# Kernel tuning notes

Hardware: AMD Instinct MI355X
Metric: run time of the kernel (lower is better)

## Reference

```python
import jax, jax.numpy as jnp
from jax import lax
import numpy as np

DIM = 768
NUM_HEADS = 12
HEAD_DIM = DIM // NUM_HEADS
POOL = 8
LAM1_INIT = 0.5
LAM2_INIT = 0.5
EPS = 1e-6


def rmsnorm(x, w):
    # x / (||x||_2 / sqrt(d) + eps) * w
    d = x.shape[-1]
    rms = jnp.sqrt(jnp.sum(x * x, axis=-1, keepdims=True)) / jnp.sqrt(jnp.asarray(d, x.dtype))
    return x / (rms + EPS) * w


def setup_inputs() -> dict:
    key = jax.random.key(0)
    ks = jax.random.split(key, 10)
    B, H, W = 32, 32, 32
    N = H * W
    x = jax.random.normal(ks[0], (B, N, DIM), dtype=jnp.float32)
    Wqkv = jax.random.normal(ks[1], (3 * DIM, DIM), dtype=jnp.float32) * 0.02
    Wproj = jax.random.normal(ks[2], (DIM, DIM), dtype=jnp.float32) * 0.02
    bproj = jnp.zeros((DIM,), dtype=jnp.float32)
    Wpos = jax.random.normal(ks[3], (HEAD_DIM, HEAD_DIM), dtype=jnp.float32) * 0.02
    Wneg = jax.random.normal(ks[4], (HEAD_DIM, HEAD_DIM), dtype=jnp.float32) * 0.02
    conv_w = jax.random.normal(ks[5], (HEAD_DIM, 1, 3, 3), dtype=jnp.float32) * 0.1  # depthwise OIHW
    lam1 = jnp.asarray(LAM1_INIT, dtype=jnp.float32)
    lam2 = jnp.asarray(LAM2_INIT, dtype=jnp.float32)
    norm1_w = jnp.ones((HEAD_DIM,), dtype=jnp.float32)
    norm2_w = jnp.ones((HEAD_DIM,), dtype=jnp.float32)
    return {"x": x, "Wqkv": Wqkv, "Wproj": Wproj, "bproj": bproj, "Wpos": Wpos,
            "Wneg": Wneg, "conv_w": conv_w, "lam1": lam1, "lam2": lam2,
            "norm1_w": norm1_w, "norm2_w": norm2_w, "H": H, "W": W}


def reference(x, Wqkv, Wproj, bproj, Wpos, Wneg, conv_w, lam1, lam2, norm1_w, norm2_w, H, W):
    B, N, C = x.shape
    h, hd, p = NUM_HEADS, HEAD_DIM, POOL
    scale = hd ** -0.5
    # qkv projection -> [3, B, h, N, hd]
    qkv = (x @ Wqkv.T).reshape(B, N, 3, h, hd).transpose(2, 0, 3, 1, 4)
    q, k, v = qkv[0], qkv[1], qkv[2]
    # depthwise conv + GELU on q in spatial form
    q2 = q.reshape(B, h, H, W, hd).transpose(0, 1, 4, 2, 3).reshape(B * h, hd, H, W)
    qe = lax.conv_general_dilated(q2, conv_w, window_strides=(1, 1), padding='SAME',
                                  feature_group_count=hd,
                                  dimension_numbers=('NCHW', 'OIHW', 'NCHW'))
    qe = jax.nn.gelu(qe, approximate=False)
    # adaptive avg pool to (p, p): exact since H % p == 0
    qp = qe.reshape(B * h, hd, p, H // p, p, W // p).mean(axis=(3, 5))
    t_base = qp.reshape(B, h, hd, p, p).transpose(0, 1, 3, 4, 2).reshape(B, h, p * p, hd)
    # dynamic e+/e- embeddings from global query
    gq = q.mean(axis=2)  # [B, h, hd]
    t_pos = t_base + (gq @ Wpos.T)[:, :, None, :]
    t_neg = t_base + (gq @ Wneg.T)[:, :, None, :]
    # stage 1: pooled contrast tokens attend to k/v
    attn_pos = jax.nn.softmax(jnp.einsum('bhmd,bhnd->bhmn', t_pos, k) * scale, axis=-1)
    v_hat_pos = attn_pos @ v  # [B, h, p*p, hd]
    attn_neg = jax.nn.softmax(jnp.einsum('bhmd,bhnd->bhmn', t_neg, k) * scale, axis=-1)
    v_hat_neg = attn_neg @ v
    v_contrast = rmsnorm(v_hat_pos - lam1 * v_hat_neg, norm1_w) * (1.0 - LAM1_INIT)
    # stage 2: q attends to contrast tokens
    attn1 = jax.nn.softmax(jnp.einsum('bhnd,bhmd->bhnm', q, t_pos) * scale, axis=-1)
    attn2 = jax.nn.softmax(jnp.einsum('bhnd,bhmd->bhnm', q, t_neg) * scale, axis=-1)
    out_patch = (attn1 - lam2 * attn2) @ v_contrast  # [B, h, N, hd]
    out_patch = rmsnorm(out_patch, norm2_w) * (1.0 - LAM2_INIT)
    out_patch = out_patch.transpose(0, 2, 1, 3).reshape(B, N, C)
    out = out_patch @ Wproj.T + bproj
    return out
```

## Files before the change

kernel.cpp:

```cpp
#include <hip/hip_runtime.h>
#include <hip/hip_bf16.h>


typedef __attribute__((ext_vector_type(8))) short short8;
typedef __attribute__((ext_vector_type(4))) short bf16x4;
typedef __attribute__((ext_vector_type(4))) float f32x4;

#define DEV static __device__ __forceinline__

DEV unsigned short f2bf(float f) {
  unsigned int b; __builtin_memcpy(&b, &f, 4);
  unsigned int r = (b + 0x7FFFu + ((b >> 16) & 1u)) >> 16;
  return (unsigned short)r;
}
DEV float bf2f(unsigned short u) {
  unsigned int b = ((unsigned int)u) << 16;
  float f; __builtin_memcpy(&f, &b, 4);
  return f;
}

DEV void gload16(const unsigned short* g, unsigned short* l) {
  __builtin_amdgcn_global_load_lds(
      (const __attribute__((address_space(1))) unsigned int*)g,
      (__attribute__((address_space(3))) unsigned int*)l, 16, 0, 0);
}

constexpr size_t SZ_QKV = (size_t)32 * 12 * 1024 * 64 * 2;
constexpr size_t OFF_Q   = 0;
constexpr size_t OFF_K   = OFF_Q + SZ_QKV;
constexpr size_t OFF_VT  = OFF_K + SZ_QKV;
constexpr size_t OFF_TPB = OFF_VT + SZ_QKV;
constexpr size_t OFF_TNB = OFF_TPB + 3145728;
constexpr size_t OFF_VCT = OFF_TNB + 3145728;
constexpr size_t OFF_OP  = OFF_VCT + 6291456;
constexpr size_t OFF_XB  = OFF_OP + SZ_QKV;
constexpr size_t OFF_WQ  = OFF_XB + SZ_QKV;
constexpr size_t OFF_WP  = OFF_WQ + 3538944;
constexpr size_t OFF_EP  = OFF_WP + 1179648;
constexpr size_t OFF_EN  = OFF_EP + 98304;

__global__ __launch_bounds__(256) void cast_kernel(const float* __restrict__ src,
                                                   unsigned short* __restrict__ dst, int n4) {
  int i = blockIdx.x * 256 + threadIdx.x;
  if (i >= n4) return;
  float4 v = reinterpret_cast<const float4*>(src)[i];
  ushort4 o;
  o.x = f2bf(v.x); o.y = f2bf(v.y); o.z = f2bf(v.z); o.w = f2bf(v.w);
  reinterpret_cast<ushort4*>(dst)[i] = o;
}

__global__ __launch_bounds__(256) void gemm_qkv_kernel(const unsigned short* __restrict__ A,
    const unsigned short* __restrict__ Bm, unsigned short* __restrict__ q,
    unsigned short* __restrict__ k, unsigned short* __restrict__ vt) {
  __shared__ unsigned short As[2 * 128 * 32];
  __shared__ unsigned short Bs[2 * 128 * 32];
  const int t = threadIdx.x;
  const int lane = t & 63;
  const int w = t >> 6;
  const int wm = w >> 1, wn = w & 1;
  const int row0 = blockIdx.y * 128;
  const int col0 = blockIdx.x * 128;
  f32x4 acc[4][4];
#pragma unroll
  for (int i = 0; i < 4; ++i)
#pragma unroll
    for (int j = 0; j < 4; ++j) acc[i][j] = (f32x4){0.f, 0.f, 0.f, 0.f};
  const int l = lane & 15, g = lane >> 4;
  const int srow = lane >> 2, scol = (lane & 3) << 3;
  for (int k0 = 0; k0 < 768; k0 += 64) {
    __syncthreads();
#pragma unroll
    for (int kc = 0; kc < 2; ++kc)
#pragma unroll
      for (int j = 0; j < 2; ++j) {
        const int qs = w * 2 + j;
        const int r = qs * 16 + srow;
        const int cg = k0 + kc * 32 + scol;
        gload16(A + (size_t)(row0 + r) * 768 + cg, As + kc * 4096 + qs * 512);
        gload16(Bm + (size_t)(col0 + r) * 768 + cg, Bs + kc * 4096 + qs * 512);
      }
    __syncthreads();
#pragma unroll
    for (int kc = 0; kc < 2; ++kc) {
      short8 af[4], bfv[4];
#pragma unroll
      for (int mt = 0; mt < 4; ++mt)
        af[mt] = *reinterpret_cast<const short8*>(As + kc * 4096 + (wm * 64 + mt * 16 + l) * 32 + g * 8);
#pragma unroll
      for (int nt = 0; nt < 4; ++nt)
        bfv[nt] = *reinterpret_cast<const short8*>(Bs + kc * 4096 + (wn * 64 + nt * 16 + l) * 32 + g * 8);
#pragma unroll
      for (int mt = 0; mt < 4; ++mt)
#pragma unroll
        for (int nt = 0; nt < 4; ++nt)
          acc[mt][nt] = __builtin_amdgcn_mfma_f32_16x16x32_bf16(af[mt], bfv[nt], acc[mt][nt], 0, 0, 0);
    }
  }
  const int s_ = col0 / 768;
  if (s_ == 2) {
#pragma unroll
    for (int nt = 0; nt < 4; ++nt) {
      const int colin = wn * 64 + nt * 16 + l;
      const int head = ((col0 % 768) + colin) >> 6;
      const int d = colin & 63;
#pragma unroll
      for (int mt = 0; mt < 4; ++mt) {
        const int row = row0 + wm * 64 + mt * 16 + (g << 2);
        const int b = row >> 10, n = row & 1023;
        ushort4 pk;
        pk.x = f2bf(acc[mt][nt][0]); pk.y = f2bf(acc[mt][nt][1]);
        pk.z = f2bf(acc[mt][nt][2]); pk.w = f2bf(acc[mt][nt][3]);
        *reinterpret_cast<ushort4*>(vt + ((((size_t)b * 12 + head) * 64 + d) << 10) + n) = pk;
      }
    }
  } else {
    unsigned short* dst = (s_ == 0) ? q : k;
#pragma unroll
    for (int nt = 0; nt < 4; ++nt) {
      const int colin = wn * 64 + nt * 16 + l;
      const int head = ((col0 % 768) + colin) >> 6;
      const int d = colin & 63;
#pragma unroll
      for (int mt = 0; mt < 4; ++mt) {
#pragma unroll
        for (int r = 0; r < 4; ++r) {
          const int row = row0 + wm * 64 + mt * 16 + (g << 2) + r;
          const int b = row >> 10, n = row & 1023;
          dst[(((size_t)b * 12 + head) * 1024 + n) * 64 + d] = f2bf(acc[mt][nt][r]);
        }
      }
    }
  }
}

__global__ __launch_bounds__(256) void gq_embed_kernel(const unsigned short* __restrict__ qg,
    const float* __restrict__ Wpos, const float* __restrict__ Wneg,
    float* __restrict__ ep, float* __restrict__ en) {
  const int bh = blockIdx.x;
  const unsigned short* qp = qg + (size_t)bh * 65536;
  __shared__ float red2[32][64];
  __shared__ float gq_s[64];
  const int t = threadIdx.x;
  const int c8 = (t & 7) << 3;
  const int part = t >> 3;
  float s[8] = {0.f, 0.f, 0.f, 0.f, 0.f, 0.f, 0.f, 0.f};
  for (int i = 0; i < 32; ++i) {
    const short8 v = *reinterpret_cast<const short8*>(qp + (size_t)(part * 32 + i) * 64 + c8);
#pragma unroll
    for (int j = 0; j < 8; ++j) s[j] += bf2f((unsigned short)v[j]);
  }
#pragma unroll
  for (int j = 0; j < 8; ++j) red2[part][c8 + j] = s[j];
  __syncthreads();
  if (t < 64) {
    float s2 = 0.f;
    for (int p = 0; p < 32; ++p) s2 += red2[p][t];
    gq_s[t] = s2 * (1.0f / 1024.0f);
  }
  __syncthreads();
  if (t < 128) {
    const int d2 = t & 63;
    const float* Wm = (t < 64) ? Wpos : Wneg;
    float e = 0.f;
    for (int dd = 0; dd < 64; ++dd) e += gq_s[dd] * Wm[d2 * 64 + dd];
    (t < 64 ? ep : en)[bh * 64 + d2] = e;
  }
}

__global__ __launch_bounds__(256) void conv_pool_kernel(const unsigned short* __restrict__ qg,
    const float* __restrict__ conv_w, const float* __restrict__ ep,
    const float* __restrict__ en, unsigned short* __restrict__ t_pos,
    unsigned short* __restrict__ t_neg) {
  const int bh = blockIdx.x;
  const int quad = blockIdx.y;
  const unsigned short* qp = qg + (size_t)bh * 65536;
  __shared__ float pool_s[16][64];
  const int t = threadIdx.x;
  const int dg = t & 7, sp = t >> 3;
  const int d0 = dg << 3;
  float cw[3][3][8];
#pragma unroll
  for (int ky = 0; ky < 3; ++ky)
#pragma unroll
    for (int kx = 0; kx < 3; ++kx)
#pragma unroll
      for (int j = 0; j < 8; ++j)
        cw[ky][kx][j] = conv_w[(d0 + j) * 9 + ky * 3 + kx];
#pragma unroll
  for (int pyl = 0; pyl < 2; ++pyl) {
    float win[8] = {0.f, 0.f, 0.f, 0.f, 0.f, 0.f, 0.f, 0.f};
#pragma unroll
    for (int iy = 0; iy < 4; ++iy) {
      const int y = quad * 8 + pyl * 4 + iy;
      float a[8] = {0.f, 0.f, 0.f, 0.f, 0.f, 0.f, 0.f, 0.f};
#pragma unroll
      for (int ky = 0; ky < 3; ++ky) {
        const int yy = y + ky - 1;
        if (yy < 0 || yy > 31) continue;
#pragma unroll
        for (int kx = 0; kx < 3; ++kx) {
          const int xx = sp + kx - 1;
          if (xx < 0 || xx > 31) continue;
          const short8 v = *reinterpret_cast<const short8*>(qp + (size_t)(yy * 32 + xx) * 64 + d0);
#pragma unroll
          for (int j = 0; j < 8; ++j) a[j] += bf2f((unsigned short)v[j]) * cw[ky][kx][j];
        }
      }
#pragma unroll
      for (int j = 0; j < 8; ++j)
        win[j] += 0.5f * a[j] * (1.0f + erff(a[j] * 0.70710678118654752440f));
    }
#pragma unroll
    for (int j = 0; j < 8; ++j) {
      win[j] += __shfl_xor(win[j], 8);
      win[j] += __shfl_xor(win[j], 16);
    }
    if ((sp & 3) == 0) {
      const int px = sp >> 2;
#pragma unroll
      for (int j = 0; j < 8; ++j) pool_s[pyl * 8 + px][d0 + j] = win[j];
    }
  }
  __syncthreads();
#pragma unroll
  for (int i = 0; i < 4; ++i) {
    const int idx = i * 256 + t;
    const int m = idx >> 6, dd = idx & 63;
    const int mg = quad * 16 + m;
    const float base = pool_s[m][dd] * (1.0f / 16.0f);
    t_pos[(size_t)bh * 4096 + mg * 64 + dd] = f2bf(base + ep[bh * 64 + dd]);
    t_neg[(size_t)bh * 4096 + mg * 64 + dd] = f2bf(base + en[bh * 64 + dd]);
  }
}

__global__ __launch_bounds__(256) void stage1_kernel(const unsigned short* __restrict__ kg,
    const unsigned short* __restrict__ vtg, const unsigned short* __restrict__ tpb,
    const unsigned short* __restrict__ tnb, const float* __restrict__ lam1p,
    const float* __restrict__ norm1_w, float* __restrict__ vct) {
  const int bh = blockIdx.x;
  __shared__ unsigned short tp[64 * 72], tn[64 * 72];
  __shared__ unsigned short Ks[64 * 72], Vts[64 * 72];
  const int t = threadIdx.x;
  const int lane = t & 63;
  const int w = t >> 6;
  const int l = lane & 15, g = lane >> 4;
  for (int L = t; L < 512; L += 256) {
    const int r = L >> 3, c = (L & 7) << 3;
    *reinterpret_cast<short8*>(tp + r * 72 + c) =
        *reinterpret_cast<const short8*>(tpb + (size_t)bh * 4096 + r * 64 + c);
    *reinterpret_cast<short8*>(tn + r * 72 + c) =
        *reinterpret_cast<const short8*>(tnb + (size_t)bh * 4096 + r * 64 + c);
  }
  __syncthreads();
  short8 tf[2][2];
#pragma unroll
  for (int h = 0; h < 2; ++h) {
    tf[0][h] = *reinterpret_cast<const short8*>(tp + (w * 16 + l) * 72 + h * 32 + g * 8);
    tf[1][h] = *reinterpret_cast<const short8*>(tn + (w * 16 + l) * 72 + h * 32 + g * 8);
  }
  float Mo[2] = {-1e30f, -1e30f}, Lo[2] = {0.f, 0.f};
  f32x4 acc[2][4];
#pragma unroll
  for (int pp = 0; pp < 2; ++pp)
#pragma unroll
    for (int dt = 0; dt < 4; ++dt) acc[pp][dt] = (f32x4){0.f, 0.f, 0.f, 0.f};
  const size_t kbase = (size_t)bh * 65536;

  for (int n0 = 0; n0 < 1024; n0 += 64) {
    __syncthreads();
    for (int L = t; L < 512; L += 256) {
      const int r = L >> 3, c = (L & 7) << 3;
      *reinterpret_cast<short8*>(Ks + r * 72 + c) =
          *reinterpret_cast<const short8*>(kg + kbase + (size_t)(n0 + r) * 64 + c);
      *reinterpret_cast<short8*>(Vts + r * 72 + c) =
          *reinterpret_cast<const short8*>(vtg + kbase + (size_t)r * 1024 + n0 + c);
    }
    __syncthreads();
    short8 kf[4][2];
#pragma unroll
    for (int tile = 0; tile < 4; ++tile)
#pragma unroll
      for (int h = 0; h < 2; ++h)
        kf[tile][h] = *reinterpret_cast<const short8*>(Ks + (tile * 16 + l) * 72 + h * 32 + g * 8);
    bf16x4 pf[2][4];
#pragma unroll
    for (int pp = 0; pp < 2; ++pp) {
      f32x4 s[4];
#pragma unroll
      for (int tile = 0; tile < 4; ++tile) {
        s[tile] = (f32x4){0.f, 0.f, 0.f, 0.f};
#pragma unroll
        for (int h = 0; h < 2; ++h)
          s[tile] = __builtin_amdgcn_mfma_f32_16x16x32_bf16(kf[tile][h], tf[pp][h], s[tile], 0, 0, 0);
      }
      float p[4][4];
      float tmax = -1e30f;
#pragma unroll
      for (int tile = 0; tile < 4; ++tile)
#pragma unroll
        for (int r = 0; r < 4; ++r) {
          const float v = s[tile][r] * 0.125f;
          p[tile][r] = v;
          tmax = fmaxf(tmax, v);
        }
      tmax = fmaxf(tmax, __shfl_xor(tmax, 16));
      tmax = fmaxf(tmax, __shfl_xor(tmax, 32));
      const float nm = fmaxf(Mo[pp], tmax);
      const float al = __expf(Mo[pp] - nm);
      Mo[pp] = nm;
      float ps = 0.f;
#pragma unroll
      for (int tile = 0; tile < 4; ++tile)
#pragma unroll
        for (int r = 0; r < 4; ++r) {
          const float e = __expf(p[tile][r] - nm);
          p[tile][r] = e;
          ps += e;
        }
      ps += __shfl_xor(ps, 16);
      ps += __shfl_xor(ps, 32);
      Lo[pp] = Lo[pp] * al + ps;
#pragma unroll
      for (int tile = 0; tile < 4; ++tile) {
        bf16x4 pk;
        pk[0] = (short)f2bf(p[tile][0]); pk[1] = (short)f2bf(p[tile][1]);
        pk[2] = (short)f2bf(p[tile][2]); pk[3] = (short)f2bf(p[tile][3]);
        pf[pp][tile] = pk;
      }
      float ar[4];
#pragma unroll
      for (int r = 0; r < 4; ++r) ar[r] = __shfl(al, 4 * g + r);
#pragma unroll
      for (int dt = 0; dt < 4; ++dt)
#pragma unroll
        for (int r = 0; r < 4; ++r) acc[pp][dt][r] *= ar[r];
    }
#pragma unroll
    for (int tile = 0; tile < 4; ++tile)
#pragma unroll
      for (int dt = 0; dt < 4; ++dt) {
        const bf16x4 vf = *reinterpret_cast<const bf16x4*>(Vts + (dt * 16 + l) * 72 + tile * 16 + g * 4);
        acc[0][dt] = __builtin_amdgcn_mfma_f32_16x16x16bf16_1k(pf[0][tile], vf, acc[0][dt], 0, 0, 0);
        acc[1][dt] = __builtin_amdgcn_mfma_f32_16x16x16bf16_1k(pf[1][tile], vf, acc[1][dt], 0, 0, 0);
      }
  }
  const float inv0 = 1.f / Lo[0], inv1 = 1.f / Lo[1];
  float i1r[4], i2r[4];
#pragma unroll
  for (int r = 0; r < 4; ++r) {
    i1r[r] = __shfl(inv0, 4 * g + r);
    i2r[r] = __shfl(inv1, 4 * g + r);
  }
  const float lam1 = lam1p[0];
  float od[4][4], ss[4] = {0.f, 0.f, 0.f, 0.f};
#pragma unroll
  for (int dt = 0; dt < 4; ++dt)
#pragma unroll
    for (int r = 0; r < 4; ++r) {
      const float v = acc[0][dt][r] * i1r[r] - lam1 * (acc[1][dt][r] * i2r[r]);
      od[dt][r] = v;
      ss[r] += v * v;
    }
#pragma unroll
  for (int r = 0; r < 4; ++r) {
    ss[r] += __shfl_xor(ss[r], 1);
    ss[r] += __shfl_xor(ss[r], 2);
    ss[r] += __shfl_xor(ss[r], 4);
    ss[r] += __shfl_xor(ss[r], 8);
  }
  float sc[4];
#pragma unroll
  for (int r = 0; r < 4; ++r) sc[r] = 0.5f / (sqrtf(ss[r]) * 0.125f + 1e-6f);
  const int mb = w * 16 + 4 * g;
#pragma unroll
  for (int dt = 0; dt < 4; ++dt) {
    const int dd = dt * 16 + l;
    const float nw = norm1_w[dd];
#pragma unroll
    for (int r = 0; r < 4; ++r)
      vct[(size_t)bh * 4096 + dd * 64 + mb + r] = od[dt][r] * sc[r] * nw;
  }
}

__global__ __launch_bounds__(256) void stage2_kernel(const unsigned short* __restrict__ qg,
    const unsigned short* __restrict__ tpb, const unsigned short* __restrict__ tnb,
    const float* __restrict__ vct, const float* __restrict__ lam2p,
    const float* __restrict__ norm2_w, unsigned short* __restrict__ opb) {
  const int bh = blockIdx.x;
  const int q0 = blockIdx.y * 64;
  __shared__ unsigned short tp[64 * 72], tn[64 * 72], Qs[64 * 72], Vc[64 * 72];
  const int t = threadIdx.x;
  const int lane = t & 63;
  const int w = t >> 6;
  const int l = lane & 15, g = lane >> 4;
  for (int L = t; L < 512; L += 256) {
    const int r = L >> 3, c = (L & 7) << 3;
    *reinterpret_cast<short8*>(tp + r * 72 + c) =
        *reinterpret_cast<const short8*>(tpb + (size_t)bh * 4096 + r * 64 + c);
    *reinterpret_cast<short8*>(tn + r * 72 + c) =
        *reinterpret_cast<const short8*>(tnb + (size_t)bh * 4096 + r * 64 + c);
    *reinterpret_cast<short8*>(Qs + r * 72 + c) =
        *reinterpret_cast<const short8*>(qg + (size_t)bh * 65536 + (size_t)(q0 + r) * 64 + c);
  }
  for (int L = t; L < 4096; L += 256) {
    const int dd = L >> 6, m = L & 63;
    Vc[dd * 72 + m] = f2bf(vct[(size_t)bh * 4096 + L]);
  }
  __syncthreads();
  short8 qf[2];
#pragma unroll
  for (int h = 0; h < 2; ++h)
    qf[h] = *reinterpret_cast<const short8*>(Qs + (w * 16 + l) * 72 + h * 32 + g * 8);
  bf16x4 vcf[4][4];
#pragma unroll
  for (int tile = 0; tile < 4; ++tile)
#pragma unroll
    for (int dt = 0; dt < 4; ++dt)
      vcf[tile][dt] = *reinterpret_cast<const bf16x4*>(Vc + (dt * 16 + l) * 72 + tile * 16 + g * 4);
  bf16x4 pf[2][4];
#pragma unroll
  for (int pp = 0; pp < 2; ++pp) {
    const unsigned short* tm = pp ? tn : tp;
    f32x4 s[4];
#pragma unroll
    for (int tile = 0; tile < 4; ++tile) {
      s[tile] = (f32x4){0.f, 0.f, 0.f, 0.f};
#pragma unroll
      for (int h = 0; h < 2; ++h) {
        const short8 tfb = *reinterpret_cast<const short8*>(tm + (tile * 16 + l) * 72 + h * 32 + g * 8);
        s[tile] = __builtin_amdgcn_mfma_f32_16x16x32_bf16(tfb, qf[h], s[tile], 0, 0, 0);
      }
    }
    float p[4][4];
    float lmax = -1e30f;
#pragma unroll
    for (int tile = 0; tile < 4; ++tile)
#pragma unroll
      for (int r = 0; r < 4; ++r) {
        const float v = s[tile][r] * 0.125f;
        p[tile][r] = v;
        lmax = fmaxf(lmax, v);
      }
    lmax = fmaxf(lmax, __shfl_xor(lmax, 16));
    lmax = fmaxf(lmax, __shfl_xor(lmax, 32));
    float ps = 0.f;
#pragma unroll
    for (int tile = 0; tile < 4; ++tile)
#pragma unroll
      for (int r = 0; r < 4; ++r) {
        const float e = __expf(p[tile][r] - lmax);
        p[tile][r] = e;
        ps += e;
      }
    ps += __shfl_xor(ps, 16);
    ps += __shfl_xor(ps, 32);
    const float inv = 1.f / ps;
#pragma unroll
    for (int tile = 0; tile < 4; ++tile) {
      bf16x4 pk;
      pk[0] = (short)f2bf(p[tile][0] * inv); pk[1] = (short)f2bf(p[tile][1] * inv);
      pk[2] = (short)f2bf(p[tile][2] * inv); pk[3] = (short)f2bf(p[tile][3] * inv);
      pf[pp][tile] = pk;
    }
  }
  f32x4 a1[4], a2[4];
#pragma unroll
  for (int dt = 0; dt < 4; ++dt) {
    a1[dt] = (f32x4){0.f, 0.f, 0.f, 0.f};
    a2[dt] = (f32x4){0.f, 0.f, 0.f, 0.f};
  }
#pragma unroll
  for (int tile = 0; tile < 4; ++tile)
#pragma unroll
    for (int dt = 0; dt < 4; ++dt) {
      a1[dt] = __builtin_amdgcn_mfma_f32_16x16x16bf16_1k(pf[0][tile], vcf[tile][dt], a1[dt], 0, 0, 0);
      a2[dt] = __builtin_amdgcn_mfma_f32_16x16x16bf16_1k(pf[1][tile], vcf[tile][dt], a2[dt], 0, 0, 0);
    }
  const float lam2 = lam2p[0];
  float od[4][4], ss[4] = {0.f, 0.f, 0.f, 0.f};
#pragma unroll
  for (int dt = 0; dt < 4; ++dt)
#pragma unroll
    for (int r = 0; r < 4; ++r) {
      const float v = a1[dt][r] - lam2 * a2[dt][r];
      od[dt][r] = v;
      ss[r] += v * v;
    }
#pragma unroll
  for (int r = 0; r < 4; ++r) {
    ss[r] += __shfl_xor(ss[r], 1);
    ss[r] += __shfl_xor(ss[r], 2);
    ss[r] += __shfl_xor(ss[r], 4);
    ss[r] += __shfl_xor(ss[r], 8);
  }
  float sc[4];
#pragma unroll
  for (int r = 0; r < 4; ++r) sc[r] = 0.5f / (sqrtf(ss[r]) * 0.125f + 1e-6f);
  const int b = bh / 12, head = bh % 12;
  const size_t ob = ((size_t)b * 1024 + q0 + w * 16 + 4 * g) * 768 + head * 64;
#pragma unroll
  for (int dt = 0; dt < 4; ++dt) {
    const float nw = norm2_w[dt * 16 + l];
#pragma unroll
    for (int r = 0; r < 4; ++r)
      opb[ob + (size_t)r * 768 + dt * 16 + l] = f2bf(od[dt][r] * sc[r] * nw);
  }
}

__global__ __launch_bounds__(256) void gemm_proj_kernel(const unsigned short* __restrict__ A,
    const unsigned short* __restrict__ Bm, const float* __restrict__ bias,
    float* __restrict__ out) {
  __shared__ unsigned short As[2 * 128 * 32];
  __shared__ unsigned short Bs[2 * 128 * 32];
  const int t = threadIdx.x;
  const int lane = t & 63;
  const int w = t >> 6;
  const int wm = w >> 1, wn = w & 1;
  const int row0 = blockIdx.y * 128;
  const int col0 = blockIdx.x * 128;
  f32x4 acc[4][4];
#pragma unroll
  for (int i = 0; i < 4; ++i)
#pragma unroll
    for (int j = 0; j < 4; ++j) acc[i][j] = (f32x4){0.f, 0.f, 0.f, 0.f};
  const int l = lane & 15, g = lane >> 4;
  const int srow = lane >> 2, scol = (lane & 3) << 3;
  for (int k0 = 0; k0 < 768; k0 += 64) {
    __syncthreads();
#pragma unroll
    for (int kc = 0; kc < 2; ++kc)
#pragma unroll
      for (int j = 0; j < 2; ++j) {
        const int qs = w * 2 + j;
        const int r = qs * 16 + srow;
        const int cg = k0 + kc * 32 + scol;
        gload16(A + (size_t)(row0 + r) * 768 + cg, As + kc * 4096 + qs * 512);
        gload16(Bm + (size_t)(col0 + r) * 768 + cg, Bs + kc * 4096 + qs * 512);
      }
    __syncthreads();
#pragma unroll
    for (int kc = 0; kc < 2; ++kc) {
      short8 af[4], bfv[4];
#pragma unroll
      for (int mt = 0; mt < 4; ++mt)
        af[mt] = *reinterpret_cast<const short8*>(As + kc * 4096 + (wm * 64 + mt * 16 + l) * 32 + g * 8);
#pragma unroll
      for (int nt = 0; nt < 4; ++nt)
        bfv[nt] = *reinterpret_cast<const short8*>(Bs + kc * 4096 + (wn * 64 + nt * 16 + l) * 32 + g * 8);
#pragma unroll
      for (int mt = 0; mt < 4; ++mt)
#pragma unroll
        for (int nt = 0; nt < 4; ++nt)
          acc[mt][nt] = __builtin_amdgcn_mfma_f32_16x16x32_bf16(af[mt], bfv[nt], acc[mt][nt], 0, 0, 0);
    }
  }
#pragma unroll
  for (int nt = 0; nt < 4; ++nt) {
    const int col = col0 + wn * 64 + nt * 16 + l;
    const float bv = bias[col];
#pragma unroll
    for (int mt = 0; mt < 4; ++mt)
#pragma unroll
      for (int r = 0; r < 4; ++r) {
        const int row = row0 + wm * 64 + mt * 16 + (g << 2) + r;
        out[(size_t)row * 768 + col] = acc[mt][nt][r] + bv;
      }
  }
}

extern "C" void kernel_launch(void* const* d_in, const int* in_sizes, int n_in,
                              void* d_out, int out_size, void* d_ws, size_t ws_size,
                              hipStream_t stream) {
  (void)in_sizes; (void)n_in; (void)out_size; (void)ws_size;
  const float* x       = (const float*)d_in[0];
  const float* Wqkv    = (const float*)d_in[1];
  const float* Wproj   = (const float*)d_in[2];
  const float* bproj   = (const float*)d_in[3];
  const float* Wpos    = (const float*)d_in[4];
  const float* Wneg    = (const float*)d_in[5];
  const float* conv_w  = (const float*)d_in[6];
  const float* lam1    = (const float*)d_in[7];
  const float* lam2    = (const float*)d_in[8];
  const float* norm1_w = (const float*)d_in[9];
  const float* norm2_w = (const float*)d_in[10];
  float* out = (float*)d_out;
  char* ws = (char*)d_ws;
  unsigned short* qb   = (unsigned short*)(ws + OFF_Q);
  unsigned short* kb   = (unsigned short*)(ws + OFF_K);
  unsigned short* vtb  = (unsigned short*)(ws + OFF_VT);
  unsigned short* tpbb = (unsigned short*)(ws + OFF_TPB);
  unsigned short* tnbb = (unsigned short*)(ws + OFF_TNB);
  float* vctb          = (float*)(ws + OFF_VCT);
  unsigned short* opb  = (unsigned short*)(ws + OFF_OP);
  unsigned short* xb   = (unsigned short*)(ws + OFF_XB);
  unsigned short* wqb  = (unsigned short*)(ws + OFF_WQ);
  unsigned short* wpb  = (unsigned short*)(ws + OFF_WP);
  float* epb           = (float*)(ws + OFF_EP);
  float* enb           = (float*)(ws + OFF_EN);

  cast_kernel<<<dim3(6291456 / 256), dim3(256), 0, stream>>>(x, xb, 6291456);
  cast_kernel<<<dim3(442368 / 256), dim3(256), 0, stream>>>(Wqkv, wqb, 442368);
  cast_kernel<<<dim3(147456 / 256), dim3(256), 0, stream>>>(Wproj, wpb, 147456);
  gemm_qkv_kernel<<<dim3(18, 256), dim3(256), 0, stream>>>(xb, wqb, qb, kb, vtb);
  gq_embed_kernel<<<dim3(384), dim3(256), 0, stream>>>(qb, Wpos, Wneg, epb, enb);
  conv_pool_kernel<<<dim3(384, 4), dim3(256), 0, stream>>>(qb, conv_w, epb, enb, tpbb, tnbb);
  stage1_kernel<<<dim3(384), dim3(256), 0, stream>>>(kb, vtb, tpbb, tnbb, lam1, norm1_w, vctb);
  stage2_kernel<<<dim3(384, 16), dim3(256), 0, stream>>>(qb, tpbb, tnbb, vctb, lam2, norm2_w, opb);
  gemm_proj_kernel<<<dim3(6, 256), dim3(256), 0, stream>>>(opb, wpb, bproj, out);
}
```

Measured before the change: 453.9 us.

## Rewrite QKV GEMM as 256x256 pipelined tile; double-buffer projection GEMM

The QKV GEMM moves to 512-thread blocks computing 256x256 tiles. It uses an XOR-swizzled LDS layout, split half-tile async prefetch into double buffers, explicit vmcnt waits, setprio around MFMA bursts, and a swizzled 1D grid for L2 locality. The projection GEMM gains double-buffered LDS prefetch and a swizzled block order. The aim is to hide global-load latency, cut LDS bank conflicts and raise MFMA utilisation, in exchange for more registers, more LDS and tricky barrier and waitcnt ordering.

```diff
diff --git a/kernel.cpp b/kernel.cpp
--- a/kernel.cpp
+++ b/kernel.cpp
@@ -24,6 +24,14 @@
       (const __attribute__((address_space(1))) unsigned int*)g,
       (__attribute__((address_space(3))) unsigned int*)l, 16, 0, 0);
 }
+
+DEV void bar() {
+  asm volatile("" ::: "memory");
+  __builtin_amdgcn_s_barrier();
+  asm volatile("" ::: "memory");
+}
+DEV void wait_vm4() { asm volatile("s_waitcnt vmcnt(4)" ::: "memory"); __builtin_amdgcn_sched_barrier(0); }
+DEV void wait_vm0() { asm volatile("s_waitcnt vmcnt(0)" ::: "memory"); __builtin_amdgcn_sched_barrier(0); }
 
 constexpr size_t SZ_QKV = (size_t)32 * 12 * 1024 * 64 * 2;
 constexpr size_t OFF_Q   = 0;
@@ -49,84 +57,159 @@
   reinterpret_cast<ushort4*>(dst)[i] = o;
 }
 
-__global__ __launch_bounds__(256) void gemm_qkv_kernel(const unsigned short* __restrict__ A,
+DEV void stage_ht(const unsigned short* __restrict__ G, unsigned short* shbase,
+                  int grow0, int k0, int htrow0, int w, int lane) {
+  const int rl = lane >> 3;
+  const int ck = (lane & 7) ^ rl;
+  const unsigned short* s0 = G + (size_t)(grow0 + htrow0 + w * 16 + rl) * 768 + k0 + ck * 8;
+  gload16(s0, shbase + (htrow0 + w * 16) * 64);
+  gload16(s0 + (size_t)8 * 768, shbase + (htrow0 + w * 16 + 8) * 64);
+}
+
+__global__ __launch_bounds__(512, 2) void gemm_qkv_kernel(const unsigned short* __restrict__ A,
     const unsigned short* __restrict__ Bm, unsigned short* __restrict__ q,
     unsigned short* __restrict__ k, unsigned short* __restrict__ vt) {
-  __shared__ unsigned short As[2 * 128 * 32];
-  __shared__ unsigned short Bs[2 * 128 * 32];
+  __shared__ __align__(16) unsigned short sh[65536];
   const int t = threadIdx.x;
   const int lane = t & 63;
   const int w = t >> 6;
-  const int wm = w >> 1, wn = w & 1;
-  const int row0 = blockIdx.y * 128;
-  const int col0 = blockIdx.x * 128;
-  f32x4 acc[4][4];
-#pragma unroll
-  for (int i = 0; i < 4; ++i)
+  const int wm = w >> 2, wn = w & 3;
+  const int l = lane & 15, g = lane >> 4;
+  const int id = blockIdx.x;
+  const int swz = (id & 7) * 144 + (id >> 3);
+  const int rt = swz / 9, ct = swz % 9;
+  const int row0 = rt * 256, col0 = ct * 256;
+
+  f32x4 acc[8][4];
+#pragma unroll
+  for (int i = 0; i < 8; ++i)
 #pragma unroll
     for (int j = 0; j < 4; ++j) acc[i][j] = (f32x4){0.f, 0.f, 0.f, 0.f};
-  const int l = lane & 15, g = lane >> 4;
-  const int srow = lane >> 2, scol = (lane & 3) << 3;
-  for (int k0 = 0; k0 < 768; k0 += 64) {
-    __syncthreads();
+
+  stage_ht(A, sh, row0, 0, 0, w, lane);
+  stage_ht(A, sh, row0, 0, 128, w, lane);
+  stage_ht(Bm, sh + 32768, col0, 0, 0, w, lane);
+  stage_ht(Bm, sh + 32768, col0, 0, 128, w, lane);
+  stage_ht(Bm, sh + 32768 + 16384, col0, 64, 0, w, lane);
+  stage_ht(Bm, sh + 32768 + 16384, col0, 64, 128, w, lane);
+  wait_vm4();
+  bar();
+
+  for (int m = 0; m < 12; ++m) {
+    const int d = m & 1;
+    const unsigned short* Ab = sh + d * 16384;
+    const unsigned short* Bb = sh + 32768 + d * 16384;
+    short8 af[4][2], bf0[2][2], bf1[2][2];
+#pragma unroll
+    for (int mt = 0; mt < 4; ++mt)
+#pragma unroll
+      for (int kc = 0; kc < 2; ++kc) {
+        const int r = wm * 128 + 0 * 64 + mt * 16 + l;
+        af[mt][kc] = *reinterpret_cast<const short8*>(Ab + r * 64 + (((kc << 2) | g) ^ (r & 7)) * 8);
+      }
+#pragma unroll
+    for (int nt = 0; nt < 2; ++nt)
+#pragma unroll
+      for (int kc = 0; kc < 2; ++kc) {
+        const int r = wn * 64 + 0 * 32 + nt * 16 + l;
+        bf0[nt][kc] = *reinterpret_cast<const short8*>(Bb + r * 64 + (((kc << 2) | g) ^ (r & 7)) * 8);
+      }
+    if (m + 1 < 12) stage_ht(A, sh + (d ^ 1) * 16384, row0, (m + 1) * 64, 0, w, lane);
+    bar();
+    __builtin_amdgcn_s_setprio(1);
 #pragma unroll
     for (int kc = 0; kc < 2; ++kc)
 #pragma unroll
-      for (int j = 0; j < 2; ++j) {
-        const int qs = w * 2 + j;
-        const int r = qs * 16 + srow;
-        const int cg = k0 + kc * 32 + scol;
-        gload16(A + (size_t)(row0 + r) * 768 + cg, As + kc * 4096 + qs * 512);
-        gload16(Bm + (size_t)(col0 + r) * 768 + cg, Bs + kc * 4096 + qs * 512);
-      }
-    __syncthreads();
-#pragma unroll
-    for (int kc = 0; kc < 2; ++kc) {
-      short8 af[4], bfv[4];
-#pragma unroll
       for (int mt = 0; mt < 4; ++mt)
-        af[mt] = *reinterpret_cast<const short8*>(As + kc * 4096 + (wm * 64 + mt * 16 + l) * 32 + g * 8);
-#pragma unroll
-      for (int nt = 0; nt < 4; ++nt)
-        bfv[nt] = *reinterpret_cast<const short8*>(Bs + kc * 4096 + (wn * 64 + nt * 16 + l) * 32 + g * 8);
+#pragma unroll
+        for (int nt = 0; nt < 2; ++nt)
+          acc[mt][nt] = __builtin_amdgcn_mfma_f32_16x16x32_bf16(af[mt][kc], bf0[nt][kc], acc[mt][nt], 0, 0, 0);
+    __builtin_amdgcn_s_setprio(0);
+    bar();
+#pragma unroll
+    for (int nt = 0; nt < 2; ++nt)
+#pragma unroll
+      for (int kc = 0; kc < 2; ++kc) {
+        const int r = wn * 64 + 32 + nt * 16 + l;
+        bf1[nt][kc] = *reinterpret_cast<const short8*>(Bb + r * 64 + (((kc << 2) | g) ^ (r & 7)) * 8);
+      }
+    if (m + 1 < 12) stage_ht(A, sh + (d ^ 1) * 16384, row0, (m + 1) * 64, 128, w, lane);
+    bar();
+    __builtin_amdgcn_s_setprio(1);
+#pragma unroll
+    for (int kc = 0; kc < 2; ++kc)
 #pragma unroll
       for (int mt = 0; mt < 4; ++mt)
 #pragma unroll
-        for (int nt = 0; nt < 4; ++nt)
-          acc[mt][nt] = __builtin_amdgcn_mfma_f32_16x16x32_bf16(af[mt], bfv[nt], acc[mt][nt], 0, 0, 0);
-    }
-  }
-  const int s_ = col0 / 768;
+        for (int nt = 0; nt < 2; ++nt)
+          acc[mt][2 + nt] = __builtin_amdgcn_mfma_f32_16x16x32_bf16(af[mt][kc], bf1[nt][kc], acc[mt][2 + nt], 0, 0, 0);
+    __builtin_amdgcn_s_setprio(0);
+    bar();
+#pragma unroll
+    for (int mt = 0; mt < 4; ++mt)
+#pragma unroll
+      for (int kc = 0; kc < 2; ++kc) {
+        const int r = wm * 128 + 64 + mt * 16 + l;
+        af[mt][kc] = *reinterpret_cast<const short8*>(Ab + r * 64 + (((kc << 2) | g) ^ (r & 7)) * 8);
+      }
+    if (m + 2 < 12) stage_ht(Bm, sh + 32768 + d * 16384, col0, (m + 2) * 64, 0, w, lane);
+    bar();
+    __builtin_amdgcn_s_setprio(1);
+#pragma unroll
+    for (int kc = 0; kc < 2; ++kc)
+#pragma unroll
+      for (int mt = 0; mt < 4; ++mt)
+#pragma unroll
+        for (int nt = 0; nt < 2; ++nt)
+          acc[4 + mt][2 + nt] = __builtin_amdgcn_mfma_f32_16x16x32_bf16(af[mt][kc], bf1[nt][kc], acc[4 + mt][2 + nt], 0, 0, 0);
+    __builtin_amdgcn_s_setprio(0);
+    bar();
+    if (m + 2 < 12) stage_ht(Bm, sh + 32768 + d * 16384, col0, (m + 2) * 64, 128, w, lane);
+    bar();
+    __builtin_amdgcn_s_setprio(1);
+#pragma unroll
+    for (int kc = 0; kc < 2; ++kc)
+#pragma unroll
+      for (int mt = 0; mt < 4; ++mt)
+#pragma unroll
+        for (int nt = 0; nt < 2; ++nt)
+          acc[4 + mt][nt] = __builtin_amdgcn_mfma_f32_16x16x32_bf16(af[mt][kc], bf0[nt][kc], acc[4 + mt][nt], 0, 0, 0);
+    __builtin_amdgcn_s_setprio(0);
+    if (m < 11) {
+      if (m == 10) wait_vm0(); else wait_vm4();
+    }
+    bar();
+  }
+
+  const int s_ = ct / 3;
   if (s_ == 2) {
 #pragma unroll
-    for (int nt = 0; nt < 4; ++nt) {
-      const int colin = wn * 64 + nt * 16 + l;
-      const int head = ((col0 % 768) + colin) >> 6;
-      const int d = colin & 63;
-#pragma unroll
-      for (int mt = 0; mt < 4; ++mt) {
-        const int row = row0 + wm * 64 + mt * 16 + (g << 2);
+    for (int ni = 0; ni < 4; ++ni) {
+      const int colg = (ct % 3) * 256 + wn * 64 + ni * 16 + l;
+      const int head = colg >> 6, dd = colg & 63;
+#pragma unroll
+      for (int mi = 0; mi < 8; ++mi) {
+        const int row = row0 + wm * 128 + mi * 16 + (g << 2);
         const int b = row >> 10, n = row & 1023;
         ushort4 pk;
-        pk.x = f2bf(acc[mt][nt][0]); pk.y = f2bf(acc[mt][nt][1]);
-        pk.z = f2bf(acc[mt][nt][2]); pk.w = f2bf(acc[mt][nt][3]);
-        *reinterpret_cast<ushort4*>(vt + ((((size_t)b * 12 + head) * 64 + d) << 10) + n) = pk;
+        pk.x = f2bf(acc[mi][ni][0]); pk.y = f2bf(acc[mi][ni][1]);
+        pk.z = f2bf(acc[mi][ni][2]); pk.w = f2bf(acc[mi][ni][3]);
+        *reinterpret_cast<ushort4*>(vt + ((((size_t)b * 12 + head) * 64 + dd) << 10) + n) = pk;
       }
     }
   } else {
     unsigned short* dst = (s_ == 0) ? q : k;
 #pragma unroll
-    for (int nt = 0; nt < 4; ++nt) {
-      const int colin = wn * 64 + nt * 16 + l;
-      const int head = ((col0 % 768) + colin) >> 6;
-      const int d = colin & 63;
-#pragma unroll
-      for (int mt = 0; mt < 4; ++mt) {
+    for (int ni = 0; ni < 4; ++ni) {
+      const int colg = (ct % 3) * 256 + wn * 64 + ni * 16 + l;
+      const int head = colg >> 6, dd = colg & 63;
+#pragma unroll
+      for (int mi = 0; mi < 8; ++mi) {
 #pragma unroll
         for (int r = 0; r < 4; ++r) {
-          const int row = row0 + wm * 64 + mt * 16 + (g << 2) + r;
+          const int row = row0 + wm * 128 + mi * 16 + (g << 2) + r;
           const int b = row >> 10, n = row & 1023;
-          dst[(((size_t)b * 12 + head) * 1024 + n) * 64 + d] = f2bf(acc[mt][nt][r]);
+          dst[(((size_t)b * 12 + head) * 1024 + n) * 64 + dd] = f2bf(acc[mi][ni][r]);
         }
       }
     }
@@ -507,17 +590,35 @@
   }
 }
 
+DEV void stage_tile(const unsigned short* __restrict__ A,
+                    const unsigned short* __restrict__ Bm,
+                    unsigned short* As, unsigned short* Bs,
+                    int row0, int col0, int k0, int w, int srow, int scol) {
+#pragma unroll
+  for (int kc = 0; kc < 2; ++kc)
+#pragma unroll
+    for (int j = 0; j < 2; ++j) {
+      const int qs = w * 2 + j;
+      const int r = qs * 16 + srow;
+      const int cg = k0 + kc * 32 + scol;
+      gload16(A + (size_t)(row0 + r) * 768 + cg, As + kc * 4096 + qs * 512);
+      gload16(Bm + (size_t)(col0 + r) * 768 + cg, Bs + kc * 4096 + qs * 512);
+    }
+}
+
 __global__ __launch_bounds__(256) void gemm_proj_kernel(const unsigned short* __restrict__ A,
     const unsigned short* __restrict__ Bm, const float* __restrict__ bias,
     float* __restrict__ out) {
-  __shared__ unsigned short As[2 * 128 * 32];
-  __shared__ unsigned short Bs[2 * 128 * 32];
+  __shared__ unsigned short As[2][8192];
+  __shared__ unsigned short Bs[2][8192];
   const int t = threadIdx.x;
   const int lane = t & 63;
   const int w = t >> 6;
   const int wm = w >> 1, wn = w & 1;
-  const int row0 = blockIdx.y * 128;
-  const int col0 = blockIdx.x * 128;
+  const int id = blockIdx.x;
+  const int swz = (id & 7) * 192 + (id >> 3);
+  const int row0 = (swz / 6) * 128;
+  const int col0 = (swz % 6) * 128;
   f32x4 acc[4][4];
 #pragma unroll
   for (int i = 0; i < 4; ++i)
@@ -525,34 +626,29 @@
     for (int j = 0; j < 4; ++j) acc[i][j] = (f32x4){0.f, 0.f, 0.f, 0.f};
   const int l = lane & 15, g = lane >> 4;
   const int srow = lane >> 2, scol = (lane & 3) << 3;
-  for (int k0 = 0; k0 < 768; k0 += 64) {
-    __syncthreads();
-#pragma unroll
-    for (int kc = 0; kc < 2; ++kc)
-#pragma unroll
-      for (int j = 0; j < 2; ++j) {
-        const int qs = w * 2 + j;
-        const int r = qs * 16 + srow;
-        const int cg = k0 + kc * 32 + scol;
-        gload16(A + (size_t)(row0 + r) * 768 + cg, As + kc * 4096 + qs * 512);
-        gload16(Bm + (size_t)(col0 + r) * 768 + cg, Bs + kc * 4096 + qs * 512);
-      }
-    __syncthreads();
+
+  stage_tile(A, Bm, As[0], Bs[0], row0, col0, 0, w, srow, scol);
+  __syncthreads();
+  for (int kt = 0; kt < 12; ++kt) {
+    const int cur = kt & 1;
+    if (kt < 11)
+      stage_tile(A, Bm, As[cur ^ 1], Bs[cur ^ 1], row0, col0, (kt + 1) * 64, w, srow, scol);
 #pragma unroll
     for (int kc = 0; kc < 2; ++kc) {
       short8 af[4], bfv[4];
 #pragma unroll
       for (int mt = 0; mt < 4; ++mt)
-        af[mt] = *reinterpret_cast<const short8*>(As + kc * 4096 + (wm * 64 + mt * 16 + l) * 32 + g * 8);
+        af[mt] = *reinterpret_cast<const short8*>(As[cur] + kc * 4096 + (wm * 64 + mt * 16 + l) * 32 + g * 8);
 #pragma unroll
       for (int nt = 0; nt < 4; ++nt)
-        bfv[nt] = *reinterpret_cast<const short8*>(Bs + kc * 4096 + (wn * 64 + nt * 16 + l) * 32 + g * 8);
+        bfv[nt] = *reinterpret_cast<const short8*>(Bs[cur] + kc * 4096 + (wn * 64 + nt * 16 + l) * 32 + g * 8);
 #pragma unroll
       for (int mt = 0; mt < 4; ++mt)
 #pragma unroll
         for (int nt = 0; nt < 4; ++nt)
           acc[mt][nt] = __builtin_amdgcn_mfma_f32_16x16x32_bf16(af[mt], bfv[nt], acc[mt][nt], 0, 0, 0);
     }
+    __syncthreads();
   }
 #pragma unroll
   for (int nt = 0; nt < 4; ++nt) {
@@ -601,10 +697,10 @@
   cast_kernel<<<dim3(6291456 / 256), dim3(256), 0, stream>>>(x, xb, 6291456);
   cast_kernel<<<dim3(442368 / 256), dim3(256), 0, stream>>>(Wqkv, wqb, 442368);
   cast_kernel<<<dim3(147456 / 256), dim3(256), 0, stream>>>(Wproj, wpb, 147456);
-  gemm_qkv_kernel<<<dim3(18, 256), dim3(256), 0, stream>>>(xb, wqb, qb, kb, vtb);
+  gemm_qkv_kernel<<<dim3(1152), dim3(512), 0, stream>>>(xb, wqb, qb, kb, vtb);
   gq_embed_kernel<<<dim3(384), dim3(256), 0, stream>>>(qb, Wpos, Wneg, epb, enb);
   conv_pool_kernel<<<dim3(384, 4), dim3(256), 0, stream>>>(qb, conv_w, epb, enb, tpbb, tnbb);
   stage1_kernel<<<dim3(384), dim3(256), 0, stream>>>(kb, vtb, tpbb, tnbb, lam1, norm1_w, vctb);
   stage2_kernel<<<dim3(384, 16), dim3(256), 0, stream>>>(qb, tpbb, tnbb, vctb, lam2, norm2_w, opb);
-  gemm_proj_kernel<<<dim3(6, 256), dim3(256), 0, stream>>>(opb, wpb, bproj, out);
-}
+  gemm_proj_kernel<<<dim3(1536), dim3(256), 0, stream>>>(opb, wpb, bproj, out);
+}
```

Measured after the change: 435.2 us. -4.1%, faster.
